# Optimization experiments

Hardware: AMD Instinct MI355X
Metric: run time of the kernel (lower is better)

## Reference

```python
import jax, jax.numpy as jnp
import numpy as np

B, N, OUTERDIM, DIM, N_CLASSES = 2, 6000, 1024, 512, 2
HEADS, DIM_HEAD, INNER = 8, 64, 512
LANDMARKS, PINV_ITERS, KPAD = 256, 6, 16  # residual conv kernel 33 -> pad 16
SCALE = DIM_HEAD ** -0.5


def layer_norm(x, g, b, eps=1e-5):
    mu = x.mean(-1, keepdims=True)
    var = jnp.var(x, axis=-1, keepdims=True)
    return (x - mu) * jax.lax.rsqrt(var + eps) * g + b


def moore_penrose_pinv(x, iters=PINV_ITERS):
    # x: [b, h, m, m]
    abs_x = jnp.abs(x)
    col = abs_x.sum(-1)
    row = abs_x.sum(-2)
    z = jnp.swapaxes(x, -1, -2) / (jnp.max(col) * jnp.max(row))
    I = jnp.eye(x.shape[-1], dtype=x.dtype)
    for _ in range(iters):
        xz = x @ z
        z = 0.25 * z @ (13 * I - xz @ (15 * I - xz @ (7 * I - xz)))
    return z


def nystrom_attention(x, w_qkv, w_out, b_out, conv_w):
    b, n, _ = x.shape
    pad = (-n) % LANDMARKS
    xp = jnp.pad(x, ((0, 0), (pad, 0), (0, 0)))  # pad at FRONT, as in lucidrains impl
    npad = n + pad
    qkv = xp @ w_qkv.T  # [b, npad, 3*inner]
    q, k, v = [t.reshape(b, npad, HEADS, DIM_HEAD).transpose(0, 2, 1, 3)
               for t in jnp.split(qkv, 3, axis=-1)]
    q = q * SCALE
    l = npad // LANDMARKS  # tokens per landmark
    q_l = q.reshape(b, HEADS, LANDMARKS, l, DIM_HEAD).sum(3) / l
    k_l = k.reshape(b, HEADS, LANDMARKS, l, DIM_HEAD).sum(3) / l
    attn1 = jax.nn.softmax(jnp.einsum('bhid,bhjd->bhij', q, k_l), axis=-1)   # [b,h,npad,m]
    attn2 = jax.nn.softmax(jnp.einsum('bhid,bhjd->bhij', q_l, k_l), axis=-1)  # [b,h,m,m]
    attn3 = jax.nn.softmax(jnp.einsum('bhid,bhjd->bhij', q_l, k), axis=-1)    # [b,h,m,npad]
    out = (attn1 @ moore_penrose_pinv(attn2)) @ (attn3 @ v)  # [b,h,npad,d]
    # depthwise residual conv over sequence dim (per head), kernel (33,1)
    out = out + jax.lax.conv_general_dilated(
        v, conv_w, window_strides=(1, 1), padding=((KPAD, KPAD), (0, 0)),
        dimension_numbers=('NCHW', 'OIHW', 'NCHW'), feature_group_count=HEADS)
    out = out.transpose(0, 2, 1, 3).reshape(b, npad, INNER)
    out = out @ w_out.T + b_out
    return out[:, -n:]


def setup_inputs() -> dict:
    key = jax.random.key(0)
    ks = jax.random.split(key, 12)
    w = lambda k, shape: 0.02 * jax.random.normal(k, shape, dtype=jnp.float32)
    inp = {
        'data': jax.random.normal(ks[0], (B, N, OUTERDIM), dtype=jnp.float32),
        'w1': w(ks[1], (DIM, OUTERDIM)), 'b1': jnp.zeros((DIM,), jnp.float32),
        'cls_token': jax.random.normal(ks[2], (1, 1, DIM), dtype=jnp.float32),
        'ln1_g': jnp.ones((DIM,), jnp.float32), 'ln1_b': jnp.zeros((DIM,), jnp.float32),
        'qkv1_w': w(ks[3], (3 * INNER, DIM)),
        'out1_w': w(ks[4], (DIM, INNER)), 'out1_b': jnp.zeros((DIM,), jnp.float32),
        'conv1_w': w(ks[5], (HEADS, 1, 33, 1)),
        'ln2_g': jnp.ones((DIM,), jnp.float32), 'ln2_b': jnp.zeros((DIM,), jnp.float32),
        'qkv2_w': w(ks[6], (3 * INNER, DIM)),
        'out2_w': w(ks[7], (DIM, INNER)), 'out2_b': jnp.zeros((DIM,), jnp.float32),
        'conv2_w': w(ks[8], (HEADS, 1, 33, 1)),
        'lnf_g': jnp.ones((DIM,), jnp.float32), 'lnf_b': jnp.zeros((DIM,), jnp.float32),
        'w2': w(ks[9], (N_CLASSES, DIM)), 'b2': jnp.zeros((N_CLASSES,), jnp.float32),
    }
    return inp


def reference(data, w1, b1, cls_token, ln1_g, ln1_b, qkv1_w, out1_w, out1_b, conv1_w,
              ln2_g, ln2_b, qkv2_w, out2_w, out2_b, conv2_w, lnf_g, lnf_b, w2, b2):
    h = jax.nn.relu(data @ w1.T + b1)  # [B, N, DIM]
    H = h.shape[1]
    side = int(np.ceil(np.sqrt(H)))
    add = side * side - H
    h = jnp.concatenate([h, h[:, :add]], axis=1)  # square padding: 6084
    cls = jnp.broadcast_to(cls_token, (h.shape[0], 1, h.shape[2]))
    h = jnp.concatenate([cls, h], axis=1)  # +CLS: 6085
    h = h + nystrom_attention(layer_norm(h, ln1_g, ln1_b), qkv1_w, out1_w, out1_b, conv1_w)
    h = h + nystrom_attention(layer_norm(h, ln2_g, ln2_b), qkv2_w, out2_w, out2_b, conv2_w)
    h = layer_norm(h, lnf_g, lnf_b)[:, 0]
    logits = h @ w2.T + b2
    return logits
```

## Files before the change

### kernel.cpp

```cpp
#include <hip/hip_runtime.h>
#include <cstdint>
#include <cstddef>

namespace {

constexpr int DIMC  = 512;
constexpr int SEQ   = 6085;
constexpr int NPAD  = 6144;
constexpr int PADF  = 59;
constexpr int LMK   = 256;
constexpr int BHN   = 16;
constexpr int KSPL  = 16;
constexpr int MPADR = 6016;

typedef __attribute__((ext_vector_type(8))) short bf8_t;
typedef __attribute__((ext_vector_type(4))) float f4_t;

#define MFMA(a, b, c) __builtin_amdgcn_mfma_f32_16x16x32_bf16(a, b, c, 0, 0, 0)

#define SWZB(r, cu) (((((r) << 6) + ((cu) << 1))) ^ (((r) & 7) << 4))

#define GLDS16(gp, lp) __builtin_amdgcn_global_load_lds( \
    (const __attribute__((address_space(1))) void*)(gp), \
    (__attribute__((address_space(3))) void*)(lp), 16, 0, 0)

__device__ __forceinline__ ushort f2bf(float f) {
    union { float f; uint32_t u; } c{f};
    uint32_t u = c.u;
    return (ushort)((u + 0x7FFFu + ((u >> 16) & 1u)) >> 16);
}
__device__ __forceinline__ float bf2f(ushort u) {
    union { uint32_t u; float f; } c{(uint32_t)u << 16};
    return c.f;
}

__device__ __forceinline__ float waveSum(float v) {
#pragma unroll
    for (int o = 32; o > 0; o >>= 1) v += __shfl_xor(v, o, 64);
    return v;
}
__device__ __forceinline__ float waveMax(float v) {
#pragma unroll
    for (int o = 32; o > 0; o >>= 1) v = fmaxf(v, __shfl_xor(v, o, 64));
    return v;
}
__device__ __forceinline__ float blockSum256(float v, float* sm) {
    v = waveSum(v);
    __syncthreads();
    if ((threadIdx.x & 63) == 0) sm[threadIdx.x >> 6] = v;
    __syncthreads();
    return sm[0] + sm[1] + sm[2] + sm[3];
}
__device__ __forceinline__ float blockMax256(float v, float* sm) {
    v = waveMax(v);
    __syncthreads();
    if ((threadIdx.x & 63) == 0) sm[threadIdx.x >> 6] = v;
    __syncthreads();
    return fmaxf(fmaxf(sm[0], sm[1]), fmaxf(sm[2], sm[3]));
}
__device__ __forceinline__ float grpMax(float v) {
    v = fmaxf(v, __shfl_xor(v, 1, 64));
    v = fmaxf(v, __shfl_xor(v, 2, 64));
    v = fmaxf(v, __shfl_xor(v, 4, 64));
    v = fmaxf(v, __shfl_xor(v, 8, 64));
    return v;
}
__device__ __forceinline__ float grpSum(float v) {
    v += __shfl_xor(v, 1, 64);
    v += __shfl_xor(v, 2, 64);
    v += __shfl_xor(v, 4, 64);
    v += __shfl_xor(v, 8, 64);
    return v;
}

template<int EPI>
__global__ __launch_bounds__(256)
void gemm_bt(const ushort* __restrict__ A, const ushort* __restrict__ B,
             void* __restrict__ Cv, int M, int N, int K,
             int lda, int ldb, int ldc,
             long long sA, long long sB, long long sC,
             const float* __restrict__ bias, int relu,
             ushort* __restrict__ qp, ushort* __restrict__ kp,
             ushort* __restrict__ vp, ushort* __restrict__ vtp)
{
    __shared__ __align__(16) char As_s[128 * 128];
    __shared__ __align__(16) char Bs_s[128 * 128];
    const int gx = gridDim.x, gy = gridDim.y;
    const int total = gx * gy * gridDim.z;
    int flat = (blockIdx.z * gy + blockIdx.y) * gx + blockIdx.x;
    {
        int q = total >> 3, r = total & 7;
        int xcd = flat & 7, idx = flat >> 3;
        flat = (xcd < r ? xcd * (q + 1) : r * (q + 1) + (xcd - r) * q) + idx;
    }
    const int z = flat / (gx * gy);
    const int rem = flat - z * gx * gy;
    const int by = rem / gx, bx = rem - by * gx;

    const ushort* Ab = A + (size_t)z * sA;
    const ushort* Bb = B + (size_t)z * sB;
    const int row0 = by * 128, col0 = bx * 128;
    const int tid = threadIdx.x, wid = tid >> 6, lane = tid & 63;
    const int wr = wid >> 1, wc = wid & 1, lr = lane & 15, kg = lane >> 4;
    const int srow = lane >> 3, sq = lane & 7;
    f4_t acc[4][4] = {};
    for (int k0 = 0; k0 < K; k0 += 64) {
        __syncthreads();
#pragma unroll
        for (int i = 0; i < 4; ++i) {
            int r = wid * 32 + i * 8 + srow;
            int qs = sq ^ (r & 7);
            GLDS16(Ab + (size_t)(row0 + r) * lda + k0 + qs * 8,
                   As_s + (wid * 32 + i * 8) * 128);
        }
#pragma unroll
        for (int i = 0; i < 4; ++i) {
            int r = wid * 32 + i * 8 + srow;
            int qs = sq ^ (r & 7);
            GLDS16(Bb + (size_t)(col0 + r) * ldb + k0 + qs * 8,
                   Bs_s + (wid * 32 + i * 8) * 128);
        }
        asm volatile("s_waitcnt vmcnt(0)" ::: "memory");
        __syncthreads();
#pragma unroll
        for (int ks = 0; ks < 2; ++ks) {
            bf8_t af[4], bg[4];
#pragma unroll
            for (int mr = 0; mr < 4; ++mr) {
                int r = wr * 64 + mr * 16 + lr;
                af[mr] = *(const bf8_t*)(As_s + r * 128 + ((((ks << 2) | kg) ^ (r & 7)) << 4));
            }
#pragma unroll
            for (int nr = 0; nr < 4; ++nr) {
                int r = wc * 64 + nr * 16 + lr;
                bg[nr] = *(const bf8_t*)(Bs_s + r * 128 + ((((ks << 2) | kg) ^ (r & 7)) << 4));
            }
#pragma unroll
            for (int mr = 0; mr < 4; ++mr)
#pragma unroll
                for (int nr = 0; nr < 4; ++nr)
                    acc[mr][nr] = MFMA(af[mr], bg[nr], acc[mr][nr]);
        }
    }
#pragma unroll
    for (int mr = 0; mr < 4; ++mr) {
#pragma unroll
        for (int nr = 0; nr < 4; ++nr) {
#pragma unroll
            for (int r = 0; r < 4; ++r) {
                int gm = row0 + wr * 64 + mr * 16 + kg * 4 + r;
                int gn = col0 + wc * 64 + nr * 16 + lr;
                if (gm >= M || gn >= N) continue;
                float val = acc[mr][nr][r];
                if (EPI == 0) {
                    if (bias) val += bias[gn];
                    if (relu) val = fmaxf(val, 0.f);
                    ((float*)Cv)[(size_t)z * sC + (size_t)gm * ldc + gn] = val;
                } else if (EPI == 1) {
                    ((ushort*)Cv)[(size_t)z * sC + (size_t)gm * ldc + gn] = f2bf(val);
                } else {
                    int b = (gm >= NPAD) ? 1 : 0;
                    int i = gm - b * NPAD;
                    int which = gn >> 9, hh = (gn >> 6) & 7, d = gn & 63;
                    int bh = b * 8 + hh;
                    if (which == 0)
                        qp[((size_t)bh * NPAD + i) * 64 + d] = f2bf(val * 0.125f);
                    else if (which == 1)
                        kp[((size_t)bh * NPAD + i) * 64 + d] = f2bf(val);
                    else {
                        ushort bv = f2bf(val);
                        vp[((size_t)bh * NPAD + i) * 64 + d] = bv;
                        vtp[((size_t)bh * 64 + d) * NPAD + i] = bv;
                    }
                }
            }
        }
    }
}

template<int OC, int OCT, int CTD>
__global__ __launch_bounds__(256)
void gemm_nt(const ushort* __restrict__ A, const ushort* __restrict__ Bt,
             ushort* __restrict__ C, ushort* __restrict__ CT,
             float alpha, float cd, int ldC, int ldCT,
             long long sA, long long sBt, long long sC, long long sCT)
{
    __shared__ __align__(16) char As_s[64 * 512];
    __shared__ __align__(16) char Bs_s[64 * 512];
    const int z = blockIdx.z;
    const int row0 = blockIdx.y * 64, col0 = blockIdx.x * 64;
    const int tid = threadIdx.x, wid = tid >> 6, lane = tid & 63;
    const int lr = lane & 15, kg = lane >> 4;
    const ushort* Ab = A + (size_t)z * sA;
    const ushort* Bb = Bt + (size_t)z * sBt;
    const int srow8 = lane >> 5;
    const int sch = lane & 31;
#pragma unroll
    for (int i = 0; i < 8; ++i) {
        int rb = i * 8 + wid * 2 + srow8;
        int qs = sch ^ (rb & 7);
        GLDS16(Ab + (size_t)(row0 + rb) * 256 + qs * 8,
               As_s + (i * 8 + wid * 2) * 512);
    }
#pragma unroll
    for (int i = 0; i < 8; ++i) {
        int rb = i * 8 + wid * 2 + srow8;
        int qs = sch ^ (rb & 7);
        GLDS16(Bb + (size_t)(col0 + rb) * 256 + qs * 8,
               Bs_s + (i * 8 + wid * 2) * 512);
    }
    asm volatile("s_waitcnt vmcnt(0)" ::: "memory");
    __syncthreads();
    f4_t acc[4] = {};
    const int arow = wid * 16 + lr;
#pragma unroll
    for (int ks = 0; ks < 8; ++ks) {
        bf8_t af = *(const bf8_t*)(As_s + arow * 512 + (((ks * 4 + kg) ^ (arow & 7)) << 4));
#pragma unroll
        for (int j = 0; j < 4; ++j) {
            int brow = j * 16 + lr;
            bf8_t bg = *(const bf8_t*)(Bs_s + brow * 512 + (((ks * 4 + kg) ^ (brow & 7)) << 4));
            acc[j] = MFMA(af, bg, acc[j]);
        }
    }
#pragma unroll
    for (int j = 0; j < 4; ++j) {
#pragma unroll
        for (int r = 0; r < 4; ++r) {
            int gm = row0 + wid * 16 + kg * 4 + r;
            int gn = col0 + j * 16 + lr;
            float val = alpha * acc[j][r];
            if (OC) C[(size_t)z * sC + (size_t)gm * ldC + gn] = f2bf(val);
            if (OCT) CT[(size_t)z * sCT + (size_t)gn * ldCT + gm] =
                f2bf(CTD ? (((gm == gn) ? cd : 0.f) - val) : val);
        }
    }
}

__global__ __launch_bounds__(256)
void pv_splitk(const ushort* __restrict__ S, const ushort* __restrict__ vT,
               float* __restrict__ o2p)
{
    __shared__ __align__(16) char As_s[128 * 64];
    __shared__ __align__(16) char Bs_s[64 * 64];
    const int split = blockIdx.x, mt = blockIdx.y, bh = blockIdx.z;
    const int tid = threadIdx.x;
    const int wid = tid >> 6, lane = tid & 63;
    const int lr = lane & 15, kg = lane >> 4;
    const ushort* Sb = S + (size_t)bh * LMK * NPAD + (size_t)(mt * 128) * NPAD;
    const ushort* vTb = vT + (size_t)bh * 64 * NPAD;
    const int ks0 = split * (NPAD / KSPL);
    f4_t acc[2][4] = {};
    for (int k0 = ks0; k0 < ks0 + NPAD / KSPL; k0 += 32) {
#pragma unroll
        for (int p = 0; p < 2; ++p) {
            int idx = p * 256 + tid;
            int m = idx >> 2, kc = (idx & 3) * 8;
            *(bf8_t*)(As_s + SWZB(m, kc)) = *(const bf8_t*)&Sb[(size_t)m * NPAD + k0 + kc];
        }
        {
            int n = tid >> 2, kc = (tid & 3) * 8;
            *(bf8_t*)(Bs_s + SWZB(n, kc)) = *(const bf8_t*)&vTb[(size_t)n * NPAD + k0 + kc];
        }
        __syncthreads();
        bf8_t af[2], bg[4];
#pragma unroll
        for (int i = 0; i < 2; ++i)
            af[i] = *(const bf8_t*)(As_s + SWZB(wid * 32 + i * 16 + lr, kg * 8));
#pragma unroll
        for (int j = 0; j < 4; ++j)
            bg[j] = *(const bf8_t*)(Bs_s + SWZB(j * 16 + lr, kg * 8));
#pragma unroll
        for (int i = 0; i < 2; ++i)
#pragma unroll
            for (int j = 0; j < 4; ++j)
                acc[i][j] = MFMA(af[i], bg[j], acc[i][j]);
        __syncthreads();
    }
#pragma unroll
    for (int i = 0; i < 2; ++i)
#pragma unroll
        for (int j = 0; j < 4; ++j)
#pragma unroll
            for (int r = 0; r < 4; ++r) {
                int gm = mt * 128 + wid * 32 + i * 16 + kg * 4 + r;
                int gn = j * 16 + lr;
                o2p[((size_t)(split * BHN + bh) * LMK + gm) * 64 + gn] = acc[i][j][r];
            }
}

__global__ void reduce_o2(const float* __restrict__ o2p, ushort* __restrict__ o2t) {
    int idx = blockIdx.x * 256 + threadIdx.x;
    int bh = idx >> 14, m = (idx >> 6) & 255, d = idx & 63;
    float s = 0.f;
#pragma unroll
    for (int sp = 0; sp < KSPL; ++sp)
        s += o2p[((size_t)(sp * BHN + bh) << 14) + (m << 6) + d];
    o2t[((size_t)bh * 64 + d) * 256 + m] = f2bf(s);
}

__global__ __launch_bounds__(256)
void attn1_fused(const ushort* __restrict__ q, const ushort* __restrict__ kl,
                 const ushort* __restrict__ Wt, ushort* __restrict__ ot)
{
    __shared__ __align__(16) char P_s[64 * 512];
    const int mt = blockIdx.x;
    const int bh = blockIdx.y;
    const int b = bh >> 3, hh = bh & 7;
    const int tid = threadIdx.x, wid = tid >> 6, lane = tid & 63;
    const int lr = lane & 15, kg = lane >> 4;
    const int row0 = mt * 64, rowb = wid * 16;
    const ushort* qb  = q  + (size_t)bh * NPAD * 64;
    const ushort* klb = kl + (size_t)bh * LMK * 64;
    const ushort* Wtb = Wt + (size_t)bh * 128 * 256;

    f4_t acc[16];
#pragma unroll
    for (int nf = 0; nf < 16; ++nf) acc[nf] = (f4_t){0.f, 0.f, 0.f, 0.f};
#pragma unroll
    for (int ks = 0; ks < 2; ++ks) {
        bf8_t af = *(const bf8_t*)&qb[(size_t)(row0 + rowb + lr) * 64 + ks * 32 + kg * 8];
#pragma unroll
        for (int nf = 0; nf < 16; ++nf) {
            bf8_t bg = *(const bf8_t*)&klb[(size_t)(nf * 16 + lr) * 64 + ks * 32 + kg * 8];
            acc[nf] = MFMA(af, bg, acc[nf]);
        }
    }
    float inv_s[4];
    {
        float mx[4] = {-3.0e38f, -3.0e38f, -3.0e38f, -3.0e38f};
#pragma unroll
        for (int nf = 0; nf < 16; ++nf)
#pragma unroll
            for (int r = 0; r < 4; ++r) mx[r] = fmaxf(mx[r], acc[nf][r]);
#pragma unroll
        for (int r = 0; r < 4; ++r) mx[r] = grpMax(mx[r]);
        float sum[4] = {0.f, 0.f, 0.f, 0.f};
        const int rb2 = rowb + kg * 4;
        const int cc2 = (lr & 7) * 2, chi = lr >> 3;
#pragma unroll
        for (int nf = 0; nf < 16; ++nf)
#pragma unroll
            for (int r = 0; r < 4; ++r) {
                float e = __expf(acc[nf][r] - mx[r]);
                sum[r] += e;
                int row = rb2 + r;
                int chunk = (2 * nf + chi) ^ (row & 7);
                *(ushort*)(P_s + row * 512 + chunk * 16 + cc2) = f2bf(e);
            }
#pragma unroll
        for (int r = 0; r < 4; ++r) inv_s[r] = 1.f / grpSum(sum[r]);
    }
    f4_t acc2[4] = {};
#pragma unroll
    for (int kt = 0; kt < 8; ++kt) {
        int row = rowb + lr;
        int chunk = (kt * 4 + kg) ^ (row & 7);
        bf8_t af2 = *(const bf8_t*)(P_s + row * 512 + chunk * 16);
#pragma unroll
        for (int nf = 0; nf < 4; ++nf) {
            bf8_t bg = *(const bf8_t*)&Wtb[(size_t)(nf * 16 + lr) * 256 + kt * 32 + kg * 8];
            acc2[nf] = MFMA(af2, bg, acc2[nf]);
        }
    }
#pragma unroll
    for (int nf = 0; nf < 4; ++nf)
#pragma unroll
        for (int r = 0; r < 4; ++r) {
            int gm = row0 + rowb + kg * 4 + r;
            int gn = nf * 16 + lr;
            ot[((size_t)(b * NPAD + gm)) * DIMC + hh * 64 + gn] = f2bf(acc2[nf][r] * inv_s[r]);
        }
}

__global__ void cvt_bf16(const float* __restrict__ in, ushort* __restrict__ out, int n8) {
    int i = blockIdx.x * 256 + threadIdx.x;
    if (i >= n8) return;
    float4 a = ((const float4*)in)[i * 2], b = ((const float4*)in)[i * 2 + 1];
    ushort4 lo = { f2bf(a.x), f2bf(a.y), f2bf(a.z), f2bf(a.w) };
    ushort4 hi = { f2bf(b.x), f2bf(b.y), f2bf(b.z), f2bf(b.w) };
    ((ushort4*)out)[i * 2] = lo;
    ((ushort4*)out)[i * 2 + 1] = hi;
}

__global__ void extend_h(float* __restrict__ h, const float* __restrict__ cls) {
    int b = blockIdx.y, bx = blockIdx.x;
    float* hb = h + (size_t)b * SEQ * DIMC;
    for (int c = threadIdx.x; c < DIMC; c += 256) {
        if (bx == 0) hb[c] = cls[c];
        else hb[(size_t)(6000 + bx) * DIMC + c] = hb[(size_t)bx * DIMC + c];
    }
}

__global__ void zero_xp_pad(ushort* __restrict__ xp) {
    int e = blockIdx.x * 256 + threadIdx.x;
    int b = e / (PADF * DIMC);
    int rest = e - b * (PADF * DIMC);
    xp[(size_t)b * NPAD * DIMC + rest] = 0;
}

__global__ __launch_bounds__(128)
void ln_to_xp(const float* __restrict__ h, const float* __restrict__ g,
              const float* __restrict__ bb, ushort* __restrict__ xp)
{
    __shared__ float sm[2];
    int r = blockIdx.x;
    int b = r / SEQ, i = r - b * SEQ;
    int t = threadIdx.x;
    const float4* row = (const float4*)(h + (size_t)r * DIMC);
    float4 x = row[t];
    float s  = x.x + x.y + x.z + x.w;
    float sq = x.x * x.x + x.y * x.y + x.z * x.z + x.w * x.w;
    s = waveSum(s);
    sq = waveSum(sq);
    int w = t >> 6;
    if ((t & 63) == 0) sm[w] = s;
    __syncthreads();
    float S = sm[0] + sm[1];
    __syncthreads();
    if ((t & 63) == 0) sm[w] = sq;
    __syncthreads();
    float SQ = sm[0] + sm[1];
    float mu = S * (1.f / DIMC);
    float var = SQ * (1.f / DIMC) - mu * mu;
    float rs = rsqrtf(var + 1e-5f);
    float4 gg = ((const float4*)g)[t];
    float4 bv = ((const float4*)bb)[t];
    ushort4 o;
    o.x = f2bf((x.x - mu) * rs * gg.x + bv.x);
    o.y = f2bf((x.y - mu) * rs * gg.y + bv.y);
    o.z = f2bf((x.z - mu) * rs * gg.z + bv.z);
    o.w = f2bf((x.w - mu) * rs * gg.w + bv.w);
    ((ushort4*)(xp + ((size_t)b * NPAD + PADF + i) * DIMC))[t] = o;
}

__global__ void landmark_mean(const ushort* __restrict__ in, ushort* __restrict__ out) {
    int m = blockIdx.x, bh = blockIdx.y, d = threadIdx.x;
    const ushort* p = in + ((size_t)bh * NPAD + (size_t)m * (NPAD / LMK)) * 64 + d;
    float s = 0.f;
#pragma unroll
    for (int j = 0; j < NPAD / LMK; ++j) s += bf2f(p[(size_t)j * 64]);
    out[((size_t)bh * LMK + m) * 64 + d] = f2bf(s * (1.f / (NPAD / LMK)));
}

__global__ __launch_bounds__(256)
void softmax_bf_wide(ushort* __restrict__ S) {
    __shared__ float sm[4];
    ushort* p = S + (size_t)blockIdx.x * NPAD;
    int t = threadIdx.x;
    float v[24];
    float mx = -1e30f;
#pragma unroll
    for (int j = 0; j < 24; ++j) { v[j] = bf2f(p[j * 256 + t]); mx = fmaxf(mx, v[j]); }
    float bm = blockMax256(mx, sm);
    float s = 0.f;
#pragma unroll
    for (int j = 0; j < 24; ++j) { v[j] = __expf(v[j] - bm); s += v[j]; }
    float bs = blockSum256(s, sm);
    float inv = 1.f / bs;
#pragma unroll
    for (int j = 0; j < 24; ++j) p[j * 256 + t] = f2bf(v[j] * inv);
}

__global__ __launch_bounds__(256)
void softmax_bf256(ushort* __restrict__ S) {
    __shared__ float sm[4];
    ushort* p = S + (size_t)blockIdx.x * 256;
    int t = threadIdx.x;
    float v = bf2f(p[t]);
    float bm = blockMax256(v, sm);
    float e = __expf(v - bm);
    float bs = blockSum256(e, sm);
    p[t] = f2bf(e / bs);
}

__global__ __launch_bounds__(256)
void colsum_max(const ushort* __restrict__ X, float* __restrict__ scal) {
    __shared__ float sm[4];
    int bh = blockIdx.x, t = threadIdx.x;
    const ushort* Xb = X + ((size_t)bh << 16);
    float s = 0.f;
#pragma unroll 8
    for (int i = 0; i < 256; ++i) s += bf2f(Xb[(size_t)i * 256 + t]);
    float m = blockMax256(s, sm);
    if (t == 0) atomicMax((unsigned int*)scal, __float_as_uint(m));
}

__global__ void init_z(const ushort* __restrict__ X, const float* __restrict__ scal,
                       ushort* __restrict__ Z, ushort* __restrict__ Zt) {
    size_t e = (size_t)blockIdx.x * 256 + threadIdx.x;
    int c = (int)(e & 255);
    int r = (int)((e >> 8) & 255);
    size_t bh = e >> 16;
    float inv = 1.f / scal[0];
    Z[e]  = f2bf(bf2f(X[(bh << 16) + (size_t)c * 256 + r]) * inv);
    Zt[e] = f2bf(bf2f(X[e]) * inv);
}

__global__ __launch_bounds__(256)
void conv_add(const ushort* __restrict__ v, const float* __restrict__ cw,
              ushort* __restrict__ ot)
{
    __shared__ float w[33];
    __shared__ ushort vt[96][64];
    int bh = blockIdx.y;
    int b = bh >> 3, hh = bh & 7;
    int i0 = blockIdx.x * 64;
    int t = threadIdx.x;
    if (t < 33) w[t] = cw[hh * 33 + t];
    const ushort* vb = v + (size_t)bh * NPAD * 64;
    int d = t & 63;
    for (int rr = t >> 6; rr < 96; rr += 4) {
        int j = i0 - 16 + rr;
        vt[rr][d] = (j >= 0 && j < NPAD) ? vb[(size_t)j * 64 + d] : (ushort)0;
    }
    __syncthreads();
    for (int ii = t >> 6; ii < 64; ii += 4) {
        float acc = 0.f;
#pragma unroll
        for (int kk = 0; kk < 33; ++kk) acc += w[kk] * bf2f(vt[ii + kk][d]);
        size_t off = ((size_t)(b * NPAD + i0 + ii)) * DIMC + hh * 64 + d;
        ot[off] = f2bf(bf2f(ot[off]) + acc);
    }
}

__global__ void residual_add(float* __restrict__ h, const float* __restrict__ y) {
    size_t e = (size_t)blockIdx.x * 256 + threadIdx.x;
    int c = (int)(e & 511);
    size_t ri = e >> 9;
    int i = (int)(ri % SEQ);
    int b = (int)(ri / SEQ);
    h[e] += y[((size_t)b * NPAD + PADF + i) * DIMC + c];
}

__global__ __launch_bounds__(256)
void final_head(const float* __restrict__ h, const float* __restrict__ g,
                const float* __restrict__ bb, const float* __restrict__ w2,
                const float* __restrict__ b2, float* __restrict__ out)
{
    __shared__ float row[DIMC];
    __shared__ float sm[4];
    int b = blockIdx.x;
    int t = threadIdx.x;
    const float* x = h + (size_t)b * SEQ * DIMC;
    float v0 = x[t], v1 = x[t + 256];
    float S = blockSum256(v0 + v1, sm);
    float SQ = blockSum256(v0 * v0 + v1 * v1, sm);
    float mu = S * (1.f / DIMC);
    float rs = rsqrtf(SQ * (1.f / DIMC) - mu * mu + 1e-5f);
    row[t] = (v0 - mu) * rs * g[t] + bb[t];
    row[t + 256] = (v1 - mu) * rs * g[t + 256] + bb[t + 256];
    __syncthreads();
    if (t < 64) {
        float a0 = 0.f, a1 = 0.f;
        for (int idx = t; idx < DIMC; idx += 64) {
            a0 += row[idx] * w2[idx];
            a1 += row[idx] * w2[DIMC + idx];
        }
        a0 = waveSum(a0);
        a1 = waveSum(a1);
        if (t == 0) {
            out[b * 2 + 0] = a0 + b2[0];
            out[b * 2 + 1] = a1 + b2[1];
        }
    }
}

void bt(int epi, const ushort* A, const ushort* B, void* C, int M, int N, int K,
        int lda, int ldb, int ldc, long long sA, long long sB, long long sC, int batch,
        const float* bias, int relu, ushort* qp, ushort* kp, ushort* vp, ushort* vtp,
        hipStream_t s)
{
    dim3 g((N + 127) / 128, (M + 127) / 128, batch), blk(256);
    switch (epi) {
    case 0: gemm_bt<0><<<g, blk, 0, s>>>(A, B, C, M, N, K, lda, ldb, ldc, sA, sB, sC, bias, relu, qp, kp, vp, vtp); break;
    case 1: gemm_bt<1><<<g, blk, 0, s>>>(A, B, C, M, N, K, lda, ldb, ldc, sA, sB, sC, bias, relu, qp, kp, vp, vtp); break;
    default: gemm_bt<2><<<g, blk, 0, s>>>(A, B, C, M, N, K, lda, ldb, ldc, sA, sB, sC, bias, relu, qp, kp, vp, vtp); break;
    }
}

void nt(int mode, const ushort* A, const ushort* Bt, ushort* C, ushort* CT,
        float alpha, float cd, int M, int N, int ldC, int ldCT,
        long long sA, long long sBt, long long sC, long long sCT, hipStream_t s)
{
    dim3 g(N / 64, M / 64, BHN), blk(256);
    switch (mode) {
    case 0: gemm_nt<1, 1, 1><<<g, blk, 0, s>>>(A, Bt, C, CT, alpha, cd, ldC, ldCT, sA, sBt, sC, sCT); break;
    case 1: gemm_nt<0, 1, 1><<<g, blk, 0, s>>>(A, Bt, C, CT, alpha, cd, ldC, ldCT, sA, sBt, sC, sCT); break;
    case 2: gemm_nt<1, 1, 0><<<g, blk, 0, s>>>(A, Bt, C, CT, alpha, cd, ldC, ldCT, sA, sBt, sC, sCT); break;
    default: gemm_nt<0, 1, 0><<<g, blk, 0, s>>>(A, Bt, C, CT, alpha, cd, ldC, ldCT, sA, sBt, sC, sCT); break;
    }
}

struct WS {
    float *h, *scal, *o2p, *y;
    ushort *xp, *q, *k, *v, *vT, *ql, *kl;
    ushort *datab, *w1b, *qkvwb1, *qkvwb2, *outwb1, *outwb2;
    ushort *X, *Y, *TAt, *TBt, *Z0, *Z0t, *Z1, *Z1t;
    ushort *o2t, *Wt, *S, *ot;
};

void nystrom_layer(float* h, const float* lng, const float* lnb,
                   const ushort* qkvwb, const ushort* outwb, const float* outb,
                   const float* convw, const WS& w, hipStream_t s)
{
    const long long SM = (long long)LMK * LMK;
    zero_xp_pad<<<(2 * PADF * DIMC) / 256, 256, 0, s>>>(w.xp);
    ln_to_xp<<<2 * SEQ, 128, 0, s>>>(h, lng, lnb, w.xp);
    bt(2, w.xp, qkvwb, nullptr, 2 * NPAD, 3 * DIMC, DIMC, DIMC, DIMC, 0,
       0, 0, 0, 1, nullptr, 0, w.q, w.k, w.v, w.vT, s);
    landmark_mean<<<dim3(LMK, BHN), 64, 0, s>>>(w.q, w.ql);
    landmark_mean<<<dim3(LMK, BHN), 64, 0, s>>>(w.k, w.kl);
    bt(1, w.ql, w.kl, w.X, LMK, LMK, 64, 64, 64, LMK,
       (long long)LMK * 64, (long long)LMK * 64, SM, BHN,
       nullptr, 0, nullptr, nullptr, nullptr, nullptr, s);
    softmax_bf256<<<BHN * LMK, 256, 0, s>>>(w.X);
    hipMemsetAsync(w.scal, 0, 8, s);
    colsum_max<<<BHN, 256, 0, s>>>(w.X, w.scal);
    init_z<<<(BHN * LMK * LMK) / 256, 256, 0, s>>>(w.X, w.scal, w.Z0, w.Z0t);
    ushort *Zc = w.Z0, *Zct = w.Z0t, *Zn = w.Z1, *Znt = w.Z1t;
    for (int it = 0; it < 6; ++it) {
        nt(0, w.X, Zct, w.Y, w.TAt, 1.f, 7.f, LMK, LMK, 256, 256, SM, SM, SM, SM, s);
        nt(1, w.Y, w.TAt, nullptr, w.TBt, 1.f, 15.f, LMK, LMK, 256, 256, SM, SM, 0, SM, s);
        nt(1, w.Y, w.TBt, nullptr, w.TAt, 1.f, 13.f, LMK, LMK, 256, 256, SM, SM, 0, SM, s);
        nt(2, Zc, w.TAt, Zn, Znt, 0.25f, 0.f, LMK, LMK, 256, 256, SM, SM, SM, SM, s);
        ushort* t;
        t = Zc; Zc = Zn; Zn = t;
        t = Zct; Zct = Znt; Znt = t;
    }
    bt(1, w.ql, w.k, w.S, LMK, NPAD, 64, 64, 64, NPAD,
       (long long)LMK * 64, (long long)NPAD * 64, (long long)LMK * NPAD, BHN,
       nullptr, 0, nullptr, nullptr, nullptr, nullptr, s);
    softmax_bf_wide<<<BHN * LMK, 256, 0, s>>>(w.S);
    pv_splitk<<<dim3(KSPL, 2, BHN), 256, 0, s>>>(w.S, w.vT, w.o2p);
    reduce_o2<<<BHN * LMK * 64 / 256, 256, 0, s>>>(w.o2p, w.o2t);
    nt(3, Zc, w.o2t, nullptr, w.Wt, 1.f, 0.f, LMK, 64, 256, 256,
       SM, 64 * 256, 0, 128 * 256, s);
    attn1_fused<<<dim3(NPAD / 64, BHN), 256, 0, s>>>(w.q, w.kl, w.Wt, w.ot);
    conv_add<<<dim3(NPAD / 64, BHN), 256, 0, s>>>(w.v, convw, w.ot);
    bt(0, w.ot, outwb, w.y, 2 * NPAD, DIMC, DIMC, DIMC, DIMC, DIMC,
       0, 0, 0, 1, outb, 0, nullptr, nullptr, nullptr, nullptr, s);
    residual_add<<<(2 * SEQ * DIMC) / 256, 256, 0, s>>>(h, w.y);
}

}

extern "C" void kernel_launch(void* const* d_in, const int* in_sizes, int n_in,
                              void* d_out, int out_size, void* d_ws, size_t ws_size,
                              hipStream_t stream)
{
    (void)in_sizes; (void)n_in; (void)out_size;
    const float* data  = (const float*)d_in[0];
    const float* w1    = (const float*)d_in[1];
    const float* b1    = (const float*)d_in[2];
    const float* cls   = (const float*)d_in[3];
    const float* ln1g  = (const float*)d_in[4];
    const float* ln1b  = (const float*)d_in[5];
    const float* qkv1w = (const float*)d_in[6];
    const float* out1w = (const float*)d_in[7];
    const float* out1b = (const float*)d_in[8];
    const float* conv1 = (const float*)d_in[9];
    const float* ln2g  = (const float*)d_in[10];
    const float* ln2b  = (const float*)d_in[11];
    const float* qkv2w = (const float*)d_in[12];
    const float* out2w = (const float*)d_in[13];
    const float* out2b = (const float*)d_in[14];
    const float* conv2 = (const float*)d_in[15];
    const float* lnfg  = (const float*)d_in[16];
    const float* lnfb  = (const float*)d_in[17];
    const float* w2    = (const float*)d_in[18];
    const float* b2    = (const float*)d_in[19];
    float* out = (float*)d_out;

    if (ws_size < 209473792ull) return;
    char* p = (char*)d_ws;
    auto alloc = [&](size_t bytes) { char* r = p; p += (bytes + 255) & ~(size_t)255; return r; };
    WS w;
    w.h     = (float*)alloc((size_t)2 * SEQ * DIMC * 4);
    w.xp    = (ushort*)alloc((size_t)2 * NPAD * DIMC * 2);
    w.q     = (ushort*)alloc((size_t)BHN * NPAD * 64 * 2);
    w.k     = (ushort*)alloc((size_t)BHN * NPAD * 64 * 2);
    w.v     = (ushort*)alloc((size_t)BHN * NPAD * 64 * 2);
    w.vT    = (ushort*)alloc((size_t)BHN * 64 * NPAD * 2);
    w.ql    = (ushort*)alloc((size_t)BHN * LMK * 64 * 2);
    w.kl    = (ushort*)alloc((size_t)BHN * LMK * 64 * 2);
    w.scal  = (float*)alloc(256);
    w.datab = (ushort*)alloc((size_t)2 * MPADR * 1024 * 2);
    w.w1b   = (ushort*)alloc((size_t)512 * 1024 * 2);
    w.qkvwb1= (ushort*)alloc((size_t)1536 * 512 * 2);
    w.qkvwb2= (ushort*)alloc((size_t)1536 * 512 * 2);
    w.outwb1= (ushort*)alloc((size_t)512 * 512 * 2);
    w.outwb2= (ushort*)alloc((size_t)512 * 512 * 2);
    w.X     = (ushort*)alloc((size_t)BHN * LMK * LMK * 2);
    w.Y     = (ushort*)alloc((size_t)BHN * LMK * LMK * 2);
    w.TAt   = (ushort*)alloc((size_t)BHN * LMK * LMK * 2);
    w.TBt   = (ushort*)alloc((size_t)BHN * LMK * LMK * 2);
    w.Z0    = (ushort*)alloc((size_t)BHN * LMK * LMK * 2);
    w.Z0t   = (ushort*)alloc((size_t)BHN * LMK * LMK * 2);
    w.Z1    = (ushort*)alloc((size_t)BHN * LMK * LMK * 2);
    w.Z1t   = (ushort*)alloc((size_t)BHN * LMK * LMK * 2);
    w.o2p   = (float*)alloc((size_t)KSPL * BHN * LMK * 64 * 4);
    w.o2t   = (ushort*)alloc((size_t)BHN * 64 * 256 * 2);
    w.Wt    = (ushort*)alloc((size_t)BHN * 128 * 256 * 2);
    w.S     = (ushort*)alloc((size_t)BHN * LMK * NPAD * 2);
    w.y     = (float*)w.S;
    w.ot    = w.k;

    for (int b = 0; b < 2; ++b)
        cvt_bf16<<<3000, 256, 0, stream>>>(data + (size_t)b * 6000 * 1024,
                                           w.datab + (size_t)b * MPADR * 1024, 768000);
    cvt_bf16<<<256, 256, 0, stream>>>(w1, w.w1b, 65536);
    cvt_bf16<<<384, 256, 0, stream>>>(qkv1w, w.qkvwb1, 98304);
    cvt_bf16<<<384, 256, 0, stream>>>(qkv2w, w.qkvwb2, 98304);
    cvt_bf16<<<128, 256, 0, stream>>>(out1w, w.outwb1, 32768);
    cvt_bf16<<<128, 256, 0, stream>>>(out2w, w.outwb2, 32768);

    bt(0, w.datab, w.w1b, w.h + DIMC, 6000, DIMC, 1024, 1024, 1024, DIMC,
       (long long)MPADR * 1024, 0, (long long)SEQ * DIMC, 2, b1, 1,
       nullptr, nullptr, nullptr, nullptr, stream);
    extend_h<<<dim3(85, 2), 256, 0, stream>>>(w.h, cls);

    nystrom_layer(w.h, ln1g, ln1b, w.qkvwb1, w.outwb1, out1b, conv1, w, stream);
    nystrom_layer(w.h, ln2g, ln2b, w.qkvwb2, w.outwb2, out2b, conv2, w, stream);

    final_head<<<2, 256, 0, stream>>>(w.h, lnfg, lnfb, w2, b2, out);
}
```

Baseline: 896.5 us.

## Fuse attn3 softmax normalization into PV split-K and transpose V separately

Replaces the in-place wide softmax over S with a row-stats kernel that computes only the max and inverse sum. The exponentiation and normalization are then applied on the fly while pv_splitk loads S into LDS, which saves a full write pass over the large S buffer. The uncoalesced transposed V store in the QKV GEMM epilogue becomes a separate tiled LDS transpose kernel. The attn1 kernel also prefetches the next Wt fragments ahead of the MFMAs. In exchange, pv_splitk does extra exp work per element and there is one more kernel launch.

```diff
diff --git a/kernel.cpp b/kernel.cpp
--- a/kernel.cpp
+++ b/kernel.cpp
@@ -80,8 +80,7 @@
              int lda, int ldb, int ldc,
              long long sA, long long sB, long long sC,
              const float* __restrict__ bias, int relu,
-             ushort* __restrict__ qp, ushort* __restrict__ kp,
-             ushort* __restrict__ vp, ushort* __restrict__ vtp)
+             ushort* __restrict__ qp, ushort* __restrict__ kp, ushort* __restrict__ vp)
 {
     __shared__ __align__(16) char As_s[128 * 128];
     __shared__ __align__(16) char Bs_s[128 * 128];
@@ -167,15 +166,26 @@
                         qp[((size_t)bh * NPAD + i) * 64 + d] = f2bf(val * 0.125f);
                     else if (which == 1)
                         kp[((size_t)bh * NPAD + i) * 64 + d] = f2bf(val);
-                    else {
-                        ushort bv = f2bf(val);
-                        vp[((size_t)bh * NPAD + i) * 64 + d] = bv;
-                        vtp[((size_t)bh * 64 + d) * NPAD + i] = bv;
-                    }
+                    else
+                        vp[((size_t)bh * NPAD + i) * 64 + d] = f2bf(val);
                 }
             }
         }
     }
+}
+
+__global__ void transpose_v(const ushort* __restrict__ in, ushort* __restrict__ out) {
+    __shared__ ushort tile[32][33];
+    int bh = blockIdx.z;
+    int r0 = blockIdx.x * 32, c0 = blockIdx.y * 32;
+    const ushort* ib = in + (size_t)bh * NPAD * 64;
+    ushort* ob = out + (size_t)bh * 64 * NPAD;
+    int x = threadIdx.x, y = threadIdx.y;
+    for (int yy = y; yy < 32; yy += 8)
+        tile[yy][x] = ib[(size_t)(r0 + yy) * 64 + c0 + x];
+    __syncthreads();
+    for (int yy = y; yy < 32; yy += 8)
+        ob[(size_t)(c0 + yy) * NPAD + r0 + x] = tile[x][yy];
 }
 
 template<int OC, int OCT, int CTD>
@@ -238,11 +248,32 @@
 }
 
 __global__ __launch_bounds__(256)
+void row_stats(const ushort* __restrict__ S, float* __restrict__ lm,
+               float* __restrict__ li)
+{
+    __shared__ float sm[4];
+    const ushort* p = S + (size_t)blockIdx.x * NPAD;
+    int t = threadIdx.x;
+    float v[24];
+    float mx = -1e30f;
+#pragma unroll
+    for (int j = 0; j < 24; ++j) { v[j] = bf2f(p[j * 256 + t]); mx = fmaxf(mx, v[j]); }
+    float bm = blockMax256(mx, sm);
+    float s = 0.f;
+#pragma unroll
+    for (int j = 0; j < 24; ++j) s += __expf(v[j] - bm);
+    float bs = blockSum256(s, sm);
+    if (t == 0) { lm[blockIdx.x] = bm; li[blockIdx.x] = 1.f / bs; }
+}
+
+__global__ __launch_bounds__(256)
 void pv_splitk(const ushort* __restrict__ S, const ushort* __restrict__ vT,
+               const float* __restrict__ lm, const float* __restrict__ li,
                float* __restrict__ o2p)
 {
     __shared__ __align__(16) char As_s[128 * 64];
     __shared__ __align__(16) char Bs_s[64 * 64];
+    __shared__ float smax[128], sinv[128];
     const int split = blockIdx.x, mt = blockIdx.y, bh = blockIdx.z;
     const int tid = threadIdx.x;
     const int wid = tid >> 6, lane = tid & 63;
@@ -250,13 +281,24 @@
     const ushort* Sb = S + (size_t)bh * LMK * NPAD + (size_t)(mt * 128) * NPAD;
     const ushort* vTb = vT + (size_t)bh * 64 * NPAD;
     const int ks0 = split * (NPAD / KSPL);
+    if (tid < 128) {
+        smax[tid] = lm[bh * LMK + mt * 128 + tid];
+        sinv[tid] = li[bh * LMK + mt * 128 + tid];
+    }
+    __syncthreads();
     f4_t acc[2][4] = {};
     for (int k0 = ks0; k0 < ks0 + NPAD / KSPL; k0 += 32) {
 #pragma unroll
         for (int p = 0; p < 2; ++p) {
             int idx = p * 256 + tid;
             int m = idx >> 2, kc = (idx & 3) * 8;
-            *(bf8_t*)(As_s + SWZB(m, kc)) = *(const bf8_t*)&Sb[(size_t)m * NPAD + k0 + kc];
+            bf8_t raw = *(const bf8_t*)&Sb[(size_t)m * NPAD + k0 + kc];
+            float mr = smax[m], iv = sinv[m];
+            bf8_t o;
+#pragma unroll
+            for (int j = 0; j < 8; ++j)
+                o[j] = (short)f2bf(__expf(bf2f((ushort)raw[j]) - mr) * iv);
+            *(bf8_t*)(As_s + SWZB(m, kc)) = o;
         }
         {
             int n = tid >> 2, kc = (tid & 3) * 8;
@@ -352,16 +394,26 @@
         for (int r = 0; r < 4; ++r) inv_s[r] = 1.f / grpSum(sum[r]);
     }
     f4_t acc2[4] = {};
+    bf8_t bgbuf[4];
+#pragma unroll
+    for (int nf = 0; nf < 4; ++nf)
+        bgbuf[nf] = *(const bf8_t*)&Wtb[(size_t)(nf * 16 + lr) * 256 + kg * 8];
 #pragma unroll
     for (int kt = 0; kt < 8; ++kt) {
         int row = rowb + lr;
         int chunk = (kt * 4 + kg) ^ (row & 7);
         bf8_t af2 = *(const bf8_t*)(P_s + row * 512 + chunk * 16);
-#pragma unroll
-        for (int nf = 0; nf < 4; ++nf) {
-            bf8_t bg = *(const bf8_t*)&Wtb[(size_t)(nf * 16 + lr) * 256 + kt * 32 + kg * 8];
-            acc2[nf] = MFMA(af2, bg, acc2[nf]);
-        }
+        bf8_t cur[4];
+#pragma unroll
+        for (int nf = 0; nf < 4; ++nf) cur[nf] = bgbuf[nf];
+        if (kt < 7) {
+#pragma unroll
+            for (int nf = 0; nf < 4; ++nf)
+                bgbuf[nf] = *(const bf8_t*)&Wtb[(size_t)(nf * 16 + lr) * 256 + (kt + 1) * 32 + kg * 8];
+        }
+#pragma unroll
+        for (int nf = 0; nf < 4; ++nf)
+            acc2[nf] = MFMA(af2, cur[nf], acc2[nf]);
     }
 #pragma unroll
     for (int nf = 0; nf < 4; ++nf)
@@ -444,25 +496,6 @@
 }
 
 __global__ __launch_bounds__(256)
-void softmax_bf_wide(ushort* __restrict__ S) {
-    __shared__ float sm[4];
-    ushort* p = S + (size_t)blockIdx.x * NPAD;
-    int t = threadIdx.x;
-    float v[24];
-    float mx = -1e30f;
-#pragma unroll
-    for (int j = 0; j < 24; ++j) { v[j] = bf2f(p[j * 256 + t]); mx = fmaxf(mx, v[j]); }
-    float bm = blockMax256(mx, sm);
-    float s = 0.f;
-#pragma unroll
-    for (int j = 0; j < 24; ++j) { v[j] = __expf(v[j] - bm); s += v[j]; }
-    float bs = blockSum256(s, sm);
-    float inv = 1.f / bs;
-#pragma unroll
-    for (int j = 0; j < 24; ++j) p[j * 256 + t] = f2bf(v[j] * inv);
-}
-
-__global__ __launch_bounds__(256)
 void softmax_bf256(ushort* __restrict__ S) {
     __shared__ float sm[4];
     ushort* p = S + (size_t)blockIdx.x * 256;
@@ -568,14 +601,13 @@
 
 void bt(int epi, const ushort* A, const ushort* B, void* C, int M, int N, int K,
         int lda, int ldb, int ldc, long long sA, long long sB, long long sC, int batch,
-        const float* bias, int relu, ushort* qp, ushort* kp, ushort* vp, ushort* vtp,
-        hipStream_t s)
+        const float* bias, int relu, ushort* qp, ushort* kp, ushort* vp, hipStream_t s)
 {
     dim3 g((N + 127) / 128, (M + 127) / 128, batch), blk(256);
     switch (epi) {
-    case 0: gemm_bt<0><<<g, blk, 0, s>>>(A, B, C, M, N, K, lda, ldb, ldc, sA, sB, sC, bias, relu, qp, kp, vp, vtp); break;
-    case 1: gemm_bt<1><<<g, blk, 0, s>>>(A, B, C, M, N, K, lda, ldb, ldc, sA, sB, sC, bias, relu, qp, kp, vp, vtp); break;
-    default: gemm_bt<2><<<g, blk, 0, s>>>(A, B, C, M, N, K, lda, ldb, ldc, sA, sB, sC, bias, relu, qp, kp, vp, vtp); break;
+    case 0: gemm_bt<0><<<g, blk, 0, s>>>(A, B, C, M, N, K, lda, ldb, ldc, sA, sB, sC, bias, relu, qp, kp, vp); break;
+    case 1: gemm_bt<1><<<g, blk, 0, s>>>(A, B, C, M, N, K, lda, ldb, ldc, sA, sB, sC, bias, relu, qp, kp, vp); break;
+    default: gemm_bt<2><<<g, blk, 0, s>>>(A, B, C, M, N, K, lda, ldb, ldc, sA, sB, sC, bias, relu, qp, kp, vp); break;
     }
 }
 
@@ -593,7 +625,7 @@
 }
 
 struct WS {
-    float *h, *scal, *o2p, *y;
+    float *h, *scal, *o2p, *y, *lm, *li;
     ushort *xp, *q, *k, *v, *vT, *ql, *kl;
     ushort *datab, *w1b, *qkvwb1, *qkvwb2, *outwb1, *outwb2;
     ushort *X, *Y, *TAt, *TBt, *Z0, *Z0t, *Z1, *Z1t;
@@ -608,12 +640,13 @@
     zero_xp_pad<<<(2 * PADF * DIMC) / 256, 256, 0, s>>>(w.xp);
     ln_to_xp<<<2 * SEQ, 128, 0, s>>>(h, lng, lnb, w.xp);
     bt(2, w.xp, qkvwb, nullptr, 2 * NPAD, 3 * DIMC, DIMC, DIMC, DIMC, 0,
-       0, 0, 0, 1, nullptr, 0, w.q, w.k, w.v, w.vT, s);
+       0, 0, 0, 1, nullptr, 0, w.q, w.k, w.v, s);
+    transpose_v<<<dim3(NPAD / 32, 2, BHN), dim3(32, 8), 0, s>>>(w.v, w.vT);
     landmark_mean<<<dim3(LMK, BHN), 64, 0, s>>>(w.q, w.ql);
     landmark_mean<<<dim3(LMK, BHN), 64, 0, s>>>(w.k, w.kl);
     bt(1, w.ql, w.kl, w.X, LMK, LMK, 64, 64, 64, LMK,
        (long long)LMK * 64, (long long)LMK * 64, SM, BHN,
-       nullptr, 0, nullptr, nullptr, nullptr, nullptr, s);
+       nullptr, 0, nullptr, nullptr, nullptr, s);
     softmax_bf256<<<BHN * LMK, 256, 0, s>>>(w.X);
     hipMemsetAsync(w.scal, 0, 8, s);
     colsum_max<<<BHN, 256, 0, s>>>(w.X, w.scal);
@@ -630,16 +663,16 @@
     }
     bt(1, w.ql, w.k, w.S, LMK, NPAD, 64, 64, 64, NPAD,
        (long long)LMK * 64, (long long)NPAD * 64, (long long)LMK * NPAD, BHN,
-       nullptr, 0, nullptr, nullptr, nullptr, nullptr, s);
-    softmax_bf_wide<<<BHN * LMK, 256, 0, s>>>(w.S);
-    pv_splitk<<<dim3(KSPL, 2, BHN), 256, 0, s>>>(w.S, w.vT, w.o2p);
+       nullptr, 0, nullptr, nullptr, nullptr, s);
+    row_stats<<<BHN * LMK, 256, 0, s>>>(w.S, w.lm, w.li);
+    pv_splitk<<<dim3(KSPL, 2, BHN), 256, 0, s>>>(w.S, w.vT, w.lm, w.li, w.o2p);
     reduce_o2<<<BHN * LMK * 64 / 256, 256, 0, s>>>(w.o2p, w.o2t);
     nt(3, Zc, w.o2t, nullptr, w.Wt, 1.f, 0.f, LMK, 64, 256, 256,
        SM, 64 * 256, 0, 128 * 256, s);
     attn1_fused<<<dim3(NPAD / 64, BHN), 256, 0, s>>>(w.q, w.kl, w.Wt, w.ot);
     conv_add<<<dim3(NPAD / 64, BHN), 256, 0, s>>>(w.v, convw, w.ot);
     bt(0, w.ot, outwb, w.y, 2 * NPAD, DIMC, DIMC, DIMC, DIMC, DIMC,
-       0, 0, 0, 1, outb, 0, nullptr, nullptr, nullptr, nullptr, s);
+       0, 0, 0, 1, outb, 0, nullptr, nullptr, nullptr, s);
     residual_add<<<(2 * SEQ * DIMC) / 256, 256, 0, s>>>(h, w.y);
 }
 
@@ -685,6 +718,8 @@
     w.ql    = (ushort*)alloc((size_t)BHN * LMK * 64 * 2);
     w.kl    = (ushort*)alloc((size_t)BHN * LMK * 64 * 2);
     w.scal  = (float*)alloc(256);
+    w.lm    = (float*)alloc((size_t)BHN * LMK * 4);
+    w.li    = (float*)alloc((size_t)BHN * LMK * 4);
     w.datab = (ushort*)alloc((size_t)2 * MPADR * 1024 * 2);
     w.w1b   = (ushort*)alloc((size_t)512 * 1024 * 2);
     w.qkvwb1= (ushort*)alloc((size_t)1536 * 512 * 2);
@@ -717,7 +752,7 @@
 
     bt(0, w.datab, w.w1b, w.h + DIMC, 6000, DIMC, 1024, 1024, 1024, DIMC,
        (long long)MPADR * 1024, 0, (long long)SEQ * DIMC, 2, b1, 1,
-       nullptr, nullptr, nullptr, nullptr, stream);
+       nullptr, nullptr, nullptr, stream);
     extend_h<<<dim3(85, 2), 256, 0, stream>>>(w.h, cls);
 
     nystrom_layer(w.h, ln1g, ln1b, w.qkvwb1, w.outwb1, out1b, conv1, w, stream);
```

Result: no change. 893.4 us (-0.3%).
